# Optimization experiments

Measured on AMD Instinct MI355X. Metric: run time of the kernel, lower is better.

Reference implementation:

```python
import jax, jax.numpy as jnp
import numpy as np

N, E, G = 20000, 320000, 64
F_IN, HID, HEADS, EMB = 32, 64, 4, 64
NEG_SLOPE = 0.2


def _with_self_loops(edge_index, n):
    loop = jnp.arange(n, dtype=edge_index.dtype)
    src = jnp.concatenate([edge_index[0], loop])
    dst = jnp.concatenate([edge_index[1], loop])
    return src, dst


def gat_conv(x, src, dst, W, a_src, a_dst, b, heads, out_ch, n):
    # x:[n,Fin] -> h:[n,H,C]
    h = (x @ W).reshape(n, heads, out_ch)
    al_s = jnp.sum(h * a_src, axis=-1)  # [n,H]
    al_d = jnp.sum(h * a_dst, axis=-1)  # [n,H]
    e = jax.nn.leaky_relu(al_s[src] + al_d[dst], NEG_SLOPE)  # [E',H]
    m = jax.ops.segment_max(e, dst, num_segments=n)
    ex = jnp.exp(e - m[dst])
    denom = jax.ops.segment_sum(ex, dst, num_segments=n)
    alpha = ex / (denom[dst] + 1e-16)  # softmax over incoming edges
    msg = h[src] * alpha[:, :, None]  # [E',H,C]
    out = jax.ops.segment_sum(msg, dst, num_segments=n)  # [n,H,C]
    return out.reshape(n, heads * out_ch) + b


def gcn_conv(x, src, dst, W, b, n):
    deg = jax.ops.segment_sum(jnp.ones_like(src, dtype=x.dtype), dst, num_segments=n)
    dinv = jax.lax.rsqrt(jnp.maximum(deg, 1.0))
    norm = dinv[src] * dinv[dst]  # [E']
    h = x @ W
    out = jax.ops.segment_sum(h[src] * norm[:, None], dst, num_segments=n)
    return out + b


def setup_inputs() -> dict:
    key = jax.random.key(0)
    ks = jax.random.split(key, 24)
    s = 0.05
    inp = {
        'x': jax.random.normal(ks[0], (N, F_IN), dtype=jnp.float32),
        'edge_index': jax.random.randint(ks[1], (2, E), 0, N, dtype=jnp.int32),
        'batch': jnp.sort(jax.random.randint(ks[2], (N,), 0, G, dtype=jnp.int32)),
        # GAT1: 32 -> 64, heads=4
        'W1': jax.random.normal(ks[3], (F_IN, HEADS * HID), dtype=jnp.float32) * s,
        'a_src1': jax.random.normal(ks[4], (HEADS, HID), dtype=jnp.float32) * s,
        'a_dst1': jax.random.normal(ks[5], (HEADS, HID), dtype=jnp.float32) * s,
        'b1': jnp.zeros((HEADS * HID,), dtype=jnp.float32),
        # GAT2: 256 -> 64, heads=1
        'W2': jax.random.normal(ks[6], (HEADS * HID, HID), dtype=jnp.float32) * s,
        'a_src2': jax.random.normal(ks[7], (1, HID), dtype=jnp.float32) * s,
        'a_dst2': jax.random.normal(ks[8], (1, HID), dtype=jnp.float32) * s,
        'b2': jnp.zeros((HID,), dtype=jnp.float32),
        # GCN: 64 -> 32
        'Wg': jax.random.normal(ks[9], (HID, HID // 2), dtype=jnp.float32) * s,
        'bg': jnp.zeros((HID // 2,), dtype=jnp.float32),
        # anomaly head 32->32->16->1
        'A1': jax.random.normal(ks[10], (HID // 2, 32), dtype=jnp.float32) * s,
        'ba1': jnp.zeros((32,), dtype=jnp.float32),
        'A2': jax.random.normal(ks[11], (32, 16), dtype=jnp.float32) * s,
        'ba2': jnp.zeros((16,), dtype=jnp.float32),
        'A3': jax.random.normal(ks[12], (16, 1), dtype=jnp.float32) * s,
        'ba3': jnp.zeros((1,), dtype=jnp.float32),
        # graph embedding 32->64
        'Wemb': jax.random.normal(ks[13], (HID // 2, EMB), dtype=jnp.float32) * s,
        'bemb': jnp.zeros((EMB,), dtype=jnp.float32),
    }
    return inp


def reference(x, edge_index, batch, W1, a_src1, a_dst1, b1, W2, a_src2, a_dst2, b2,
              Wg, bg, A1, ba1, A2, ba2, A3, ba3, Wemb, bemb):
    n = x.shape[0]
    src, dst = _with_self_loops(edge_index, n)
    h = jax.nn.relu(gat_conv(x, src, dst, W1, a_src1, a_dst1, b1, HEADS, HID, n))
    h = jax.nn.relu(gat_conv(h, src, dst, W2, a_src2, a_dst2, b2, 1, HID, n))
    h = jax.nn.relu(gcn_conv(h, src, dst, Wg, bg, n))
    # global mean pool over graph ids
    sums = jax.ops.segment_sum(h, batch, num_segments=G)
    cnts = jax.ops.segment_sum(jnp.ones((n, 1), dtype=h.dtype), batch, num_segments=G)
    pooled = sums / jnp.maximum(cnts, 1.0)  # [G, 32]
    z = jax.nn.relu(pooled @ A1 + ba1)
    z = jax.nn.relu(z @ A2 + ba2)
    anomaly = jax.nn.sigmoid(z @ A3 + ba3)  # [G,1]
    emb = jnp.tanh(pooled @ Wemb + bemb)    # [G,64]
    return (anomaly, emb)
```

## Files before the change

kernel.cpp:

```cpp
#include <hip/hip_runtime.h>
#include <hip/hip_bf16.h>

#define NEG 0.2f

typedef short bf16x8 __attribute__((ext_vector_type(8)));
typedef float floatx4 __attribute__((ext_vector_type(4)));

__device__ __forceinline__ float leaky(float v) { return v > 0.f ? v : NEG * v; }

__device__ __forceinline__ void unpack2(unsigned w, float& lo, float& hi) {
    union { unsigned u; float f; } a, b;
    a.u = w << 16;
    b.u = w & 0xffff0000u;
    lo = a.f; hi = b.f;
}

__device__ __forceinline__ unsigned short f2bf(float f) {
    union { float f; unsigned u; } v; v.f = f;
    unsigned r = v.u + 0x7fff + ((v.u >> 16) & 1);
    return (unsigned short)(r >> 16);
}

__global__ void prelude(const float* __restrict__ x, const float* __restrict__ W1,
                        const float* __restrict__ as1, const float* __restrict__ ad1,
                        const float* __restrict__ W2, const float* __restrict__ Wg,
                        const int* __restrict__ ei,
                        unsigned* __restrict__ xbu,
                        float* __restrict__ als1, float* __restrict__ ald1,
                        unsigned short* __restrict__ W2p,
                        unsigned short* __restrict__ W1p,
                        unsigned short* __restrict__ Wgp,
                        int* __restrict__ deg, int* __restrict__ col64,
                        int n, int E, int nTB, int nFB) {
    __shared__ float xr[64][36];
    __shared__ float WaS[128];
    __shared__ float WaD[128];
    int b = blockIdx.x;
    int t = threadIdx.x;

    if (b >= nTB) {
        int fb = b - nTB;
        if (fb < nFB) {
            int i = fb * 256 + t;
            int tot = E + n;
            if (i < tot) {
                int src, dst;
                if (i < E) { src = ei[i]; dst = ei[E + i]; }
                else { src = i - E; dst = i - E; }
                int slot = atomicAdd(&deg[dst], 1);
                if (slot < 64) col64[(size_t)dst * 64 + slot] = src;
            }
        } else {
            for (int idx = t; idx < 32 * 64; idx += 256) {
                int frag = idx >> 6, lane = idx & 63;
                int ct = frag >> 3, kt = frag & 7;
                int nn = ct * 16 + (lane & 15);
                int kb = kt * 32 + (lane >> 4) * 8;
#pragma unroll
                for (int j = 0; j < 8; j++)
                    W2p[frag * 512 + lane * 8 + j] = f2bf(W2[(kb + j) * 64 + nn]);
            }
            for (int idx = t; idx < 16 * 512; idx += 256) {
                int frag = idx >> 9;
                int h = frag >> 2, nt = frag & 3;
                int pos = idx & 511;
                int lane = pos >> 3, j = pos & 7;
                int coln = lane & 15, quad = lane >> 4;
                int k = quad * 8 + j;
                W1p[idx] = f2bf(W1[k * 256 + h * 64 + nt * 16 + coln]);
            }
            for (int idx = t; idx < 4 * 512; idx += 256) {
                int frag = idx >> 9;
                int nt = frag >> 1, kt = frag & 1;
                int pos = idx & 511;
                int lane = pos >> 3, j = pos & 7;
                int coln = lane & 15, quad = lane >> 4;
                int k = kt * 32 + quad * 8 + j;
                Wgp[idx] = f2bf(Wg[k * 32 + nt * 16 + coln]);
            }
        }
        return;
    }

    int base = b * 64;
    for (int rep = 0; rep < 2; rep++) {
        int s = t + 256 * rep;
        int node = s >> 3, quad = s & 7;
        float4 v = make_float4(0.f, 0.f, 0.f, 0.f);
        if (base + node < n) v = ((const float4*)(x + (size_t)base * 32))[s];
        *((float4*)(&xr[node][quad * 4])) = v;
    }
    {
        int j = (t & 127) >> 2, h = t & 3;
        const float* av = (t < 128) ? as1 : ad1;
        float s_ = 0.f;
#pragma unroll 8
        for (int c = 0; c < 64; c++) s_ += W1[j * 256 + h * 64 + c] * av[h * 64 + c];
        if (t < 128) WaS[t] = s_; else WaD[t - 128] = s_;
    }
    __syncthreads();

    for (int rep = 0; rep < 2; rep++) {
        int q = t + 256 * rep;
        int node = q >> 3, r = q & 7, h = r >> 1, sd = r & 1;
        int gnode = base + node;
        if (gnode < n) {
            const float* cf = sd ? WaD : WaS;
            float d_ = 0.f;
#pragma unroll
            for (int j = 0; j < 32; j++) d_ += xr[node][j] * cf[j * 4 + h];
            if (sd == 0) als1[(size_t)gnode * 4 + h] = d_;
            else         ald1[(size_t)gnode * 4 + h] = d_;
        }
    }
    for (int rep = 0; rep < 4; rep++) {
        int i = t + 256 * rep;
        int node = i >> 4, cp = i & 15;
        int gnode = base + node;
        if (gnode < n) {
            unsigned short u0 = f2bf(xr[node][cp * 2]);
            unsigned short u1 = f2bf(xr[node][cp * 2 + 1]);
            xbu[(size_t)gnode * 16 + cp] = ((unsigned)u1 << 16) | u0;
        }
    }
}

__global__ __launch_bounds__(512) void gat1_agg_mfma(
        const unsigned* __restrict__ xbu,
        const float* __restrict__ als1, const float* __restrict__ ald1,
        const int* __restrict__ deg, const int* __restrict__ col64,
        const float* __restrict__ b1,
        const unsigned short* __restrict__ W1p,
        const unsigned short* __restrict__ W2p,
        const float* __restrict__ asr, const float* __restrict__ adt,
        __hip_bfloat16* __restrict__ h2b,
        float* __restrict__ als, float* __restrict__ ald,
        float* __restrict__ dinv, int n) {
    __shared__ unsigned short xs[16 * 264];
    __shared__ unsigned short agx[16 * 136];
    __shared__ float aps[4][16];
    __shared__ float apd[4][16];
    __shared__ float ewL[1024 * 4];
    __shared__ int   colL[1024];
    int t = threadIdx.x;
    int w = t >> 6, lane = t & 63;
    int base = blockIdx.x * 16;

    for (int rep = 0; rep < 2; rep++) {
        int idx = t + 512 * rep;
        int r = idx >> 6, e = idx & 63;
        int dst = base + r;
        int s = 0;
        float4 w4 = make_float4(0.f, 0.f, 0.f, 0.f);
        if (dst < n) {
            int dgf = deg[dst];
            int dg = dgf < 64 ? dgf : 64;
            if (e < dg) {
                s = col64[(size_t)dst * 64 + e];
                float4 as4 = ((const float4*)als1)[s];
                float4 ad4 = ((const float4*)ald1)[dst];
                w4.x = __expf(leaky(as4.x + ad4.x));
                w4.y = __expf(leaky(as4.y + ad4.y));
                w4.z = __expf(leaky(as4.z + ad4.z));
                w4.w = __expf(leaky(as4.w + ad4.w));
            }
        }
        colL[idx] = s;
        *((float4*)&ewL[idx * 4]) = w4;
    }
    __syncthreads();

    {
        int h = lane >> 4, cp = lane & 15;
        for (int rep = 0; rep < 2; rep++) {
            int r = w * 2 + rep;
            int dst = base + r;
            if (dst < n) {
                int dgf = deg[dst];
                int dg = dgf < 64 ? dgf : 64;
                int dgp = (dg + 7) & ~7;
                float a0 = 0.f, a1 = 0.f, ws = 0.f;
                for (int ib = 0; ib < dgp; ib += 8) {
                    int ss[8]; float wv[8];
#pragma unroll
                    for (int u = 0; u < 8; u++) {
                        int i = r * 64 + ib + u;
                        ss[u] = colL[i];
                        wv[u] = ewL[i * 4 + h];
                    }
                    float lo[8], hi[8];
#pragma unroll
                    for (int u = 0; u < 8; u++) {
                        unsigned xv = xbu[(size_t)ss[u] * 16 + cp];
                        unpack2(xv, lo[u], hi[u]);
                    }
#pragma unroll
                    for (int u = 0; u < 8; u++) {
                        a0 += lo[u] * wv[u];
                        a1 += hi[u] * wv[u];
                        ws += wv[u];
                    }
                }
                float inv = 1.0f / (ws + 1e-16f);
                unsigned short p0 = f2bf(a0 * inv), p1 = f2bf(a1 * inv);
                *(unsigned*)(agx + r * 136 + h * 32 + cp * 2) =
                    ((unsigned)p1 << 16) | p0;
            } else {
                *(unsigned*)(agx + r * 136 + h * 32 + cp * 2) = 0u;
            }
        }
    }
    __syncthreads();

    if (w < 4) {
        int h = w;
        int mm = lane & 15, quad = lane >> 4;
        bf16x8 a = *((const bf16x8*)(agx + mm * 136 + h * 32 + quad * 8));
#pragma unroll
        for (int nt = 0; nt < 4; nt++) {
            bf16x8 bfr = *((const bf16x8*)(W1p + (h * 4 + nt) * 512 + lane * 8));
            floatx4 c = {0.f, 0.f, 0.f, 0.f};
            c = __builtin_amdgcn_mfma_f32_16x16x32_bf16(a, bfr, c, 0, 0, 0);
            int ch = h * 64 + nt * 16 + mm;
            float bb = b1[ch];
#pragma unroll
            for (int q = 0; q < 4; q++) {
                int node = quad * 4 + q;
                xs[node * 264 + ch] = f2bf(fmaxf(c[q] + bb, 0.f));
            }
        }
    }
    __syncthreads();

    if (w < 4) {
        int m = lane & 15, quad = lane >> 4;
        floatx4 acc = {0.f, 0.f, 0.f, 0.f};
#pragma unroll
        for (int kt = 0; kt < 8; kt++) {
            bf16x8 a = *((const bf16x8*)(xs + m * 264 + kt * 32 + quad * 8));
            bf16x8 b = *((const bf16x8*)(W2p + (w * 8 + kt) * 512 + lane * 8));
            acc = __builtin_amdgcn_mfma_f32_16x16x32_bf16(a, b, acc, 0, 0, 0);
        }
        int colg = w * 16 + m;
        float a_s = asr[colg], a_d = adt[colg];
        float ps[4], pd[4];
#pragma unroll
        for (int q = 0; q < 4; q++) {
            int node = base + quad * 4 + q;
            if (node < n) h2b[(size_t)node * 64 + colg] = __float2bfloat16(acc[q]);
            ps[q] = acc[q] * a_s;
            pd[q] = acc[q] * a_d;
#pragma unroll
            for (int off = 1; off <= 8; off <<= 1) {
                ps[q] += __shfl_xor(ps[q], off);
                pd[q] += __shfl_xor(pd[q], off);
            }
            if (m == 0) {
                aps[w][quad * 4 + q] = ps[q];
                apd[w][quad * 4 + q] = pd[q];
            }
        }
    }
    __syncthreads();
    if (t < 16 && base + t < n) {
        als[base + t] = aps[0][t] + aps[1][t] + aps[2][t] + aps[3][t];
        ald[base + t] = apd[0][t] + apd[1][t] + apd[2][t] + apd[3][t];
        dinv[base + t] = rsqrtf(fmaxf((float)deg[base + t], 1.0f));
    }
}

__global__ __launch_bounds__(512) void gat2_agg_mfma_gcn(
        const unsigned short* __restrict__ h2b,
        const float* __restrict__ als2, const float* __restrict__ ald2,
        const int* __restrict__ deg, const int* __restrict__ col64,
        const float* __restrict__ b2,
        const unsigned short* __restrict__ Wgp,
        unsigned short* __restrict__ h3b, int n) {
    __shared__ unsigned short h2L[16 * 72];
    __shared__ float ewL2[1024];
    __shared__ int   colL2[1024];
    int t = threadIdx.x;
    int w = t >> 6, lane = t & 63;
    int base = blockIdx.x * 16;
    int eg = lane >> 3, cl = lane & 7;

    for (int rep = 0; rep < 2; rep++) {
        int idx = t + 512 * rep;
        int r = idx >> 6, e = idx & 63;
        int dst = base + r;
        int s = 0; float wv = 0.f;
        if (dst < n) {
            int dgf = deg[dst];
            int dg = dgf < 64 ? dgf : 64;
            if (e < dg) {
                s = col64[(size_t)dst * 64 + e];
                wv = __expf(leaky(als2[s] + ald2[dst]));
            }
        }
        colL2[idx] = s;
        ewL2[idx] = wv;
    }
    __syncthreads();

    for (int rep = 0; rep < 2; rep++) {
        int r = w * 2 + rep;
        int dst = base + r;
        if (dst < n) {
            int dgf = deg[dst];
            int dg = dgf < 64 ? dgf : 64;
            float acc[8];
#pragma unroll
            for (int j = 0; j < 8; j++) acc[j] = 0.f;
            float wsum = 0.f;
            for (int ib = 0; ib < dg; ib += 16) {
                int i0 = r * 64 + ib + eg, i1 = r * 64 + ib + 8 + eg;
                int s0 = colL2[i0], s1 = colL2[i1];
                float w0 = ewL2[i0], w1 = ewL2[i1];
                uint4 hv0 = *((const uint4*)(h2b + (size_t)s0 * 64) + cl);
                uint4 hv1 = *((const uint4*)(h2b + (size_t)s1 * 64) + cl);
                wsum += w0 + w1;
                float l0, u0, l1, u1, l2, u2, l3, u3;
                unpack2(hv0.x, l0, u0); unpack2(hv0.y, l1, u1);
                unpack2(hv0.z, l2, u2); unpack2(hv0.w, l3, u3);
                acc[0] += l0 * w0; acc[1] += u0 * w0;
                acc[2] += l1 * w0; acc[3] += u1 * w0;
                acc[4] += l2 * w0; acc[5] += u2 * w0;
                acc[6] += l3 * w0; acc[7] += u3 * w0;
                unpack2(hv1.x, l0, u0); unpack2(hv1.y, l1, u1);
                unpack2(hv1.z, l2, u2); unpack2(hv1.w, l3, u3);
                acc[0] += l0 * w1; acc[1] += u0 * w1;
                acc[2] += l1 * w1; acc[3] += u1 * w1;
                acc[4] += l2 * w1; acc[5] += u2 * w1;
                acc[6] += l3 * w1; acc[7] += u3 * w1;
            }
#pragma unroll
            for (int off = 8; off <= 32; off <<= 1) {
                wsum += __shfl_xor(wsum, off);
#pragma unroll
                for (int j = 0; j < 8; j++) acc[j] += __shfl_xor(acc[j], off);
            }
            float inv = 1.0f / (wsum + 1e-16f);
            if (lane < 8) {
                const float* bb = b2 + cl * 8;
                unsigned short pk[8];
#pragma unroll
                for (int j = 0; j < 8; j++)
                    pk[j] = f2bf(fmaxf(acc[j] * inv + bb[j], 0.f));
                *((uint4*)(h2L + r * 72 + cl * 8)) = *(const uint4*)pk;
            }
        } else if (lane < 8) {
            unsigned short z[8] = {0, 0, 0, 0, 0, 0, 0, 0};
            *((uint4*)(h2L + r * 72 + cl * 8)) = *(const uint4*)z;
        }
    }
    __syncthreads();

    if (w < 2) {
        int m = lane & 15, quad = lane >> 4;
        floatx4 acc = {0.f, 0.f, 0.f, 0.f};
#pragma unroll
        for (int kt = 0; kt < 2; kt++) {
            bf16x8 a = *((const bf16x8*)(h2L + m * 72 + kt * 32 + quad * 8));
            bf16x8 bfr = *((const bf16x8*)(Wgp + (w * 2 + kt) * 512 + lane * 8));
            acc = __builtin_amdgcn_mfma_f32_16x16x32_bf16(a, bfr, acc, 0, 0, 0);
        }
#pragma unroll
        for (int q = 0; q < 4; q++) {
            int node = base + quad * 4 + q;
            if (node < n) h3b[(size_t)node * 32 + w * 16 + m] = f2bf(acc[q]);
        }
    }
}

__global__ void gcn_agg_pool(const unsigned short* __restrict__ h3b,
                             const float* __restrict__ dinv,
                             const int* __restrict__ deg, const int* __restrict__ col64,
                             const float* __restrict__ bg, const int* __restrict__ batch,
                             float* __restrict__ pooled, int n) {
    __shared__ float rowL[16][32];
    __shared__ int gL[16];
    __shared__ int   colL3[1024];
    __shared__ float nwL3[1024];
    int t = threadIdx.x;
    int w = t >> 6, lane = t & 63;
    int base = blockIdx.x * 16;

    for (int rep = 0; rep < 4; rep++) {
        int idx = t + 256 * rep;
        int r = idx >> 6, e = idx & 63;
        int dst = base + r;
        int s = 0; float nw = 0.f;
        if (dst < n) {
            int dgf = deg[dst];
            int dg = dgf < 64 ? dgf : 64;
            if (e < dg) {
                s = col64[(size_t)dst * 64 + e];
                nw = dinv[s] * dinv[dst];
            }
        }
        colL3[idx] = s;
        nwL3[idx] = nw;
    }
    __syncthreads();

    int eg = lane >> 3, cl = lane & 7;
    for (int rep = 0; rep < 4; rep++) {
        int r = w * 4 + rep;
        int dst = base + r;
        if (dst < n) {
            int dgf = deg[dst];
            int dg = dgf < 64 ? dgf : 64;
            float4 acc = make_float4(0.f, 0.f, 0.f, 0.f);
            for (int ib = 0; ib < dg; ib += 16) {
                int i0 = r * 64 + ib + eg, i1 = r * 64 + ib + 8 + eg;
                int s0 = colL3[i0], s1 = colL3[i1];
                float n0 = nwL3[i0], n1 = nwL3[i1];
                uint2 hv0 = *((const uint2*)(h3b + (size_t)s0 * 32) + cl);
                uint2 hv1 = *((const uint2*)(h3b + (size_t)s1 * 32) + cl);
                float l0, u0, l1, u1;
                unpack2(hv0.x, l0, u0); unpack2(hv0.y, l1, u1);
                acc.x += l0 * n0; acc.y += u0 * n0;
                acc.z += l1 * n0; acc.w += u1 * n0;
                unpack2(hv1.x, l0, u0); unpack2(hv1.y, l1, u1);
                acc.x += l0 * n1; acc.y += u0 * n1;
                acc.z += l1 * n1; acc.w += u1 * n1;
            }
#pragma unroll
            for (int off = 8; off <= 32; off <<= 1) {
                acc.x += __shfl_xor(acc.x, off);
                acc.y += __shfl_xor(acc.y, off);
                acc.z += __shfl_xor(acc.z, off);
                acc.w += __shfl_xor(acc.w, off);
            }
            if (lane == 0) gL[r] = batch[dst];
            if (lane < 8) {
                float4 bb = ((const float4*)bg)[cl];
                float4 o;
                o.x = fmaxf(acc.x + bb.x, 0.f);
                o.y = fmaxf(acc.y + bb.y, 0.f);
                o.z = fmaxf(acc.z + bb.z, 0.f);
                o.w = fmaxf(acc.w + bb.w, 0.f);
                *((float4*)&rowL[r][cl * 4]) = o;
            }
        } else if (lane == 0) {
            gL[r] = -1;
        }
    }
    __syncthreads();
    if (t < 32) {
        float cur = 0.f; int curg = -1;
#pragma unroll
        for (int r = 0; r < 16; r++) {
            int g = gL[r];
            if (g < 0) continue;
            float v = rowL[r][t];
            if (g == curg) cur += v;
            else {
                if (curg >= 0) atomicAdd(&pooled[curg * 32 + t], cur);
                curg = g; cur = v;
            }
        }
        if (curg >= 0) atomicAdd(&pooled[curg * 32 + t], cur);
    }
}

__device__ __forceinline__ int lbound(const int* __restrict__ b, int n, int key) {
    int lo = 0, hi = n;
    while (lo < hi) { int m = (lo + hi) >> 1; if (b[m] < key) lo = m + 1; else hi = m; }
    return lo;
}

__global__ void head_kernel(const float* __restrict__ pooled_s,
                            const int* __restrict__ batch, int n,
                            const float* __restrict__ A1, const float* __restrict__ ba1,
                            const float* __restrict__ A2, const float* __restrict__ ba2,
                            const float* __restrict__ A3, const float* __restrict__ ba3,
                            const float* __restrict__ Wemb, const float* __restrict__ bemb,
                            float* __restrict__ out) {
    __shared__ float P[64 * 32];
    __shared__ float Z1[64 * 32];
    __shared__ float Z2[64 * 16];
    __shared__ int cntL[64];
    int t = threadIdx.x;
    if (t < 64) cntL[t] = lbound(batch, n, t + 1) - lbound(batch, n, t);
    __syncthreads();
    for (int i = t; i < 64 * 32; i += 256) {
        int g = i >> 5;
        P[i] = pooled_s[i] / fmaxf((float)cntL[g], 1.0f);
    }
    __syncthreads();
    for (int i = t; i < 64 * 32; i += 256) {
        int g = i >> 5, c = i & 31;
        float a = ba1[c];
#pragma unroll
        for (int k = 0; k < 32; k++) a += P[g * 32 + k] * A1[k * 32 + c];
        Z1[i] = a > 0.f ? a : 0.f;
    }
    __syncthreads();
    for (int i = t; i < 64 * 16; i += 256) {
        int g = i >> 4, c = i & 15;
        float a = ba2[c];
#pragma unroll
        for (int k = 0; k < 32; k++) a += Z1[g * 32 + k] * A2[k * 16 + c];
        Z2[i] = a > 0.f ? a : 0.f;
    }
    __syncthreads();
    for (int g = t; g < 64; g += 256) {
        float a = ba3[0];
#pragma unroll
        for (int k = 0; k < 16; k++) a += Z2[g * 16 + k] * A3[k];
        out[g] = 1.0f / (1.0f + expf(-a));
    }
    for (int i = t; i < 64 * 64; i += 256) {
        int g = i >> 6, c = i & 63;
        float a = bemb[c];
#pragma unroll
        for (int k = 0; k < 32; k++) a += P[g * 32 + k] * Wemb[k * 64 + c];
        out[64 + i] = tanhf(a);
    }
}

extern "C" void kernel_launch(void* const* d_in, const int* in_sizes, int n_in,
                              void* d_out, int out_size, void* d_ws, size_t ws_size,
                              hipStream_t stream) {
    const float* x    = (const float*)d_in[0];
    const int*   ei   = (const int*)d_in[1];
    const int*   batch= (const int*)d_in[2];
    const float* W1   = (const float*)d_in[3];
    const float* as1  = (const float*)d_in[4];
    const float* ad1  = (const float*)d_in[5];
    const float* b1   = (const float*)d_in[6];
    const float* W2   = (const float*)d_in[7];
    const float* as2  = (const float*)d_in[8];
    const float* ad2  = (const float*)d_in[9];
    const float* b2   = (const float*)d_in[10];
    const float* Wg   = (const float*)d_in[11];
    const float* bg   = (const float*)d_in[12];
    const float* A1   = (const float*)d_in[13];
    const float* ba1  = (const float*)d_in[14];
    const float* A2   = (const float*)d_in[15];
    const float* ba2  = (const float*)d_in[16];
    const float* A3   = (const float*)d_in[17];
    const float* ba3  = (const float*)d_in[18];
    const float* Wemb = (const float*)d_in[19];
    const float* bemb = (const float*)d_in[20];
    float* out = (float*)d_out;

    const int N = in_sizes[0] / 32;
    const int E = in_sizes[1] / 2;
    const int ET = E + N;

    char* base = (char*)d_ws;
    size_t off = 0;
    auto take = [&](size_t bytes) -> char* {
        char* p = base + off;
        off = (off + bytes + 255) & ~(size_t)255;
        return p;
    };
    int*   deg    = (int*)take((size_t)N * 4);
    float* pooled = (float*)take(64 * 32 * 4);
    size_t zspan  = off;
    int*   col64  = (int*)take((size_t)N * 64 * 4);
    float* dinv   = (float*)take((size_t)N * 4);
    float* als1   = (float*)take((size_t)N * 16);
    float* ald1   = (float*)take((size_t)N * 16);
    unsigned short* W2p = (unsigned short*)take(32 * 512 * 2);
    unsigned short* W1p = (unsigned short*)take(16 * 512 * 2);
    unsigned short* Wgp = (unsigned short*)take(4 * 512 * 2);
    unsigned* xbu = (unsigned*)take((size_t)N * 64);
    __hip_bfloat16* h2b = (__hip_bfloat16*)take((size_t)N * 128);
    float* als2 = (float*)take((size_t)N * 4);
    float* ald2 = (float*)take((size_t)N * 4);
    unsigned short* h3b = (unsigned short*)take((size_t)N * 64);

    int gN16 = (N + 15) / 16;
    int gT = (N + 63) / 64;
    int gF = (ET + 255) / 256;
    int gPre = gT + gF + 1;

    hipMemsetAsync(d_ws, 0, zspan, stream);

    prelude<<<gPre, 256, 0, stream>>>(x, W1, as1, ad1, W2, Wg, ei, xbu,
                                      als1, ald1, W2p, W1p, Wgp, deg, col64,
                                      N, E, gT, gF);
    gat1_agg_mfma<<<gN16, 512, 0, stream>>>(xbu, als1, ald1, deg, col64, b1,
                                            W1p, W2p, as2, ad2,
                                            h2b, als2, ald2, dinv, N);
    gat2_agg_mfma_gcn<<<gN16, 512, 0, stream>>>((const unsigned short*)h2b,
                                                als2, ald2, deg, col64, b2,
                                                Wgp, h3b, N);
    gcn_agg_pool<<<gN16, 256, 0, stream>>>(h3b, dinv, deg, col64, bg, batch,
                                           pooled, N);
    head_kernel<<<1, 256, 0, stream>>>(pooled, batch, N, A1, ba1, A2, ba2, A3, ba3,
                                       Wemb, bemb, out);
}
```

Measured before the change: 182.0 us.

## Split GAT1 neighbor gather across lane groups with cross-lane shuffle reduction

```diff
diff --git a/kernel.cpp b/kernel.cpp
--- a/kernel.cpp
+++ b/kernel.cpp
@@ -140,8 +140,8 @@
     __shared__ unsigned short agx[16 * 136];
     __shared__ float aps[4][16];
     __shared__ float apd[4][16];
-    __shared__ float ewL[1024 * 4];
-    __shared__ int   colL[1024];
+    __shared__ float4 ewL4[1024];
+    __shared__ int    colL[1024];
     int t = threadIdx.x;
     int w = t >> 6, lane = t & 63;
     int base = blockIdx.x * 16;
@@ -166,47 +166,61 @@
             }
         }
         colL[idx] = s;
-        *((float4*)&ewL[idx * 4]) = w4;
+        ewL4[idx] = w4;
     }
     __syncthreads();
 
     {
-        int h = lane >> 4, cp = lane & 15;
+        int e4 = lane >> 4, cp = lane & 15;
         for (int rep = 0; rep < 2; rep++) {
             int r = w * 2 + rep;
             int dst = base + r;
+            floatx4 acc0 = {0.f, 0.f, 0.f, 0.f};
+            floatx4 acc1 = {0.f, 0.f, 0.f, 0.f};
+            floatx4 wsv  = {0.f, 0.f, 0.f, 0.f};
             if (dst < n) {
                 int dgf = deg[dst];
                 int dg = dgf < 64 ? dgf : 64;
                 int dgp = (dg + 7) & ~7;
-                float a0 = 0.f, a1 = 0.f, ws = 0.f;
                 for (int ib = 0; ib < dgp; ib += 8) {
-                    int ss[8]; float wv[8];
-#pragma unroll
-                    for (int u = 0; u < 8; u++) {
-                        int i = r * 64 + ib + u;
-                        ss[u] = colL[i];
-                        wv[u] = ewL[i * 4 + h];
-                    }
-                    float lo[8], hi[8];
-#pragma unroll
-                    for (int u = 0; u < 8; u++) {
-                        unsigned xv = xbu[(size_t)ss[u] * 16 + cp];
-                        unpack2(xv, lo[u], hi[u]);
-                    }
-#pragma unroll
-                    for (int u = 0; u < 8; u++) {
-                        a0 += lo[u] * wv[u];
-                        a1 += hi[u] * wv[u];
-                        ws += wv[u];
+#pragma unroll
+                    for (int u = 0; u < 2; u++) {
+                        int i = r * 64 + ib + u * 4 + e4;
+                        int s = colL[i];
+                        float4 w4 = ewL4[i];
+                        unsigned xv = xbu[(size_t)s * 16 + cp];
+                        float lo, hi;
+                        unpack2(xv, lo, hi);
+                        acc0[0] += lo * w4.x; acc1[0] += hi * w4.x;
+                        acc0[1] += lo * w4.y; acc1[1] += hi * w4.y;
+                        acc0[2] += lo * w4.z; acc1[2] += hi * w4.z;
+                        acc0[3] += lo * w4.w; acc1[3] += hi * w4.w;
+                        wsv[0] += w4.x; wsv[1] += w4.y;
+                        wsv[2] += w4.z; wsv[3] += w4.w;
                     }
                 }
-                float inv = 1.0f / (ws + 1e-16f);
-                unsigned short p0 = f2bf(a0 * inv), p1 = f2bf(a1 * inv);
-                *(unsigned*)(agx + r * 136 + h * 32 + cp * 2) =
+            }
+#pragma unroll
+            for (int off = 16; off <= 32; off <<= 1) {
+#pragma unroll
+                for (int c = 0; c < 4; c++) {
+                    acc0[c] += __shfl_xor(acc0[c], off);
+                    acc1[c] += __shfl_xor(acc1[c], off);
+                    wsv[c]  += __shfl_xor(wsv[c],  off);
+                }
+            }
+            if (dst < n) {
+                float a0s, a1s, wss;
+                if (e4 == 0)      { a0s = acc0[0]; a1s = acc1[0]; wss = wsv[0]; }
+                else if (e4 == 1) { a0s = acc0[1]; a1s = acc1[1]; wss = wsv[1]; }
+                else if (e4 == 2) { a0s = acc0[2]; a1s = acc1[2]; wss = wsv[2]; }
+                else              { a0s = acc0[3]; a1s = acc1[3]; wss = wsv[3]; }
+                float inv = 1.0f / (wss + 1e-16f);
+                unsigned short p0 = f2bf(a0s * inv), p1 = f2bf(a1s * inv);
+                *(unsigned*)(agx + r * 136 + e4 * 32 + cp * 2) =
                     ((unsigned)p1 << 16) | p0;
             } else {
-                *(unsigned*)(agx + r * 136 + h * 32 + cp * 2) = 0u;
+                *(unsigned*)(agx + r * 136 + e4 * 32 + cp * 2) = 0u;
             }
         }
     }
```

Result: slower. 186.0 us (+2.2%).
